# Performance work log

Hardware: AMD Instinct MI355X
Metric: run time of the kernel (lower is better)

## Reference

```python
import jax, jax.numpy as jnp
import numpy as np

R = 5.0  # public goods enhancement factor (init arg r)


def _neighbor_sum(x):
    # circular-padded conv2d with plus-shaped kernel [[0,1,0],[1,1,1],[0,1,0]]
    # == self + 4 von Neumann neighbors with wraparound
    return (x
            + jnp.roll(x, 1, axis=0) + jnp.roll(x, -1, axis=0)
            + jnp.roll(x, 1, axis=1) + jnp.roll(x, -1, axis=1))


def setup_inputs() -> dict:
    key = jax.random.key(0)
    ks = jax.random.split(key, 5)
    L, H = 2048, 64
    state = jax.random.randint(ks[0], (L, L), 0, 2, dtype=jnp.int32)
    s = 0.1
    return {
        "state": state,
        "W1": jax.random.normal(ks[1], (3, H), dtype=jnp.float32) * s,
        "b1": jnp.zeros((H,), dtype=jnp.float32),
        "W2": jax.random.normal(ks[2], (H, H), dtype=jnp.float32) * s,
        "b2": jnp.zeros((H,), dtype=jnp.float32),
        "Wa": jax.random.normal(ks[3], (H, 2), dtype=jnp.float32) * s,
        "ba": jnp.zeros((2,), dtype=jnp.float32),
        "Wc": jax.random.normal(ks[4], (H, 1), dtype=jnp.float32) * s,
        "bc": jnp.zeros((1,), dtype=jnp.float32),
    }


def reference(state, W1, b1, W2, b2, Wa, ba, Wc, bc):
    sf = state.astype(jnp.float32)                      # [L, L]

    # --- calculate_reward ---
    nc = _neighbor_sum(sf)                              # neighbor_coop [L, L]
    c_single = R * nc / 5.0 - 1.0
    d_single = R * nc / 5.0
    c_total = _neighbor_sum(c_single) + c_single
    d_total = _neighbor_sum(d_single) + d_single
    reward = jnp.where(state.astype(bool), c_total, d_total)  # [L, L]

    # --- encode_state ---
    global_coop = jnp.mean(sf)
    feats = jnp.stack(
        [sf, nc, jnp.broadcast_to(global_coop, sf.shape)], axis=-1
    ).reshape(-1, 3)                                    # [L*L, 3]

    # --- ActorCritic ---
    h = jax.nn.relu(feats @ W1 + b1)
    h = jax.nn.relu(h @ W2 + b2)
    action_probs = jax.nn.softmax(h @ Wa + ba, axis=-1)  # [L*L, 2]
    state_value = (h @ Wc + bc).squeeze(-1)              # [L*L]
    return action_probs, state_value, reward
```

## Files before the change

### kernel.cpp

```cpp
#include <hip/hip_runtime.h>
#include <math.h>

#define L 2048
#define LMASK (L - 1)
#define LB 512
#define LBMASK (LB - 1)
#define NCELL (L * L)
#define H 64

#define RED_BLOCKS 256
#define RED_THREADS 256
#define RED_ITERS (NCELL / 4 / (RED_BLOCKS * RED_THREADS))

__global__ void reduce_sum_kernel(const int* __restrict__ state,
                                  int* __restrict__ partials) {
    const int4* s4 = (const int4*)state;
    int tid = blockIdx.x * blockDim.x + threadIdx.x;
    int x = 0;
    #pragma unroll
    for (int k = 0; k < RED_ITERS; ++k) {
        int4 v = s4[tid + k * (RED_BLOCKS * RED_THREADS)];
        x += v.x + v.y + v.z + v.w;
    }
    #pragma unroll
    for (int off = 32; off > 0; off >>= 1)
        x += __shfl_down(x, off, 64);
    __shared__ int ls[4];
    if ((threadIdx.x & 63) == 0) ls[threadIdx.x >> 6] = x;
    __syncthreads();
    if (threadIdx.x == 0)
        partials[blockIdx.x] = ls[0] + ls[1] + ls[2] + ls[3];
}

__global__ void mlp_table_kernel(const float* __restrict__ W1,
                                 const float* __restrict__ b1,
                                 const float* __restrict__ W2,
                                 const float* __restrict__ b2,
                                 const float* __restrict__ Wa,
                                 const float* __restrict__ ba,
                                 const float* __restrict__ Wc,
                                 const float* __restrict__ bc,
                                 const int* __restrict__ partials,
                                 float* __restrict__ table) {
    __shared__ float h1[H];
    __shared__ float h2[H];
    int b = blockIdx.x;
    int j = threadIdx.x;

    int sum = partials[j] + partials[j + 64] + partials[j + 128] + partials[j + 192];
    #pragma unroll
    for (int off = 32; off > 0; off >>= 1)
        sum += __shfl_xor(sum, off, 64);

    float f0 = (float)(b / 6);
    float f1 = (float)(b % 6);
    float f2 = (float)sum * (1.0f / (float)NCELL);

    float a = W1[0 * H + j] * f0 + W1[1 * H + j] * f1 + W1[2 * H + j] * f2 + b1[j];
    h1[j] = fmaxf(a, 0.0f);
    __syncthreads();

    float acc = b2[j];
    #pragma unroll
    for (int k = 0; k < H; ++k) acc += h1[k] * W2[k * H + j];
    h2[j] = fmaxf(acc, 0.0f);
    __syncthreads();

    if (j == 0) {
        float la = ba[0], lb = ba[1], v = bc[0];
        #pragma unroll
        for (int k = 0; k < H; ++k) {
            la += h2[k] * Wa[k * 2 + 0];
            lb += h2[k] * Wa[k * 2 + 1];
            v  += h2[k] * Wc[k];
        }
        float m = fmaxf(la, lb);
        float e0 = expf(la - m), e1 = expf(lb - m);
        float inv = 1.0f / (e0 + e1);
        table[b * 4 + 0] = e0 * inv;
        table[b * 4 + 1] = e1 * inv;
        table[b * 4 + 2] = v;
    }
}

__global__ void cell_kernel(const int* __restrict__ state,
                            const float* __restrict__ table,
                            float* __restrict__ out) {
    __shared__ float tbl[48];
    if (threadIdx.x < 48) tbl[threadIdx.x] = table[threadIdx.x];
    __syncthreads();

    int tid = blockIdx.x * blockDim.x + threadIdx.x;
    int i  = tid >> 9;
    int jb = tid & LBMASK;
    int im1 = (i - 1) & LMASK, ip1 = (i + 1) & LMASK;
    int im2 = (i - 2) & LMASK, ip2 = (i + 2) & LMASK;
    int jbm1 = (jb - 1) & LBMASK, jbp1 = (jb + 1) & LBMASK;

    const int4* s4 = (const int4*)state;
    int4 m0 = s4[i   * LB + jbm1], m1 = s4[i   * LB + jb], m2 = s4[i   * LB + jbp1];
    int4 n0 = s4[im1 * LB + jbm1], n1 = s4[im1 * LB + jb], n2 = s4[im1 * LB + jbp1];
    int4 q0 = s4[ip1 * LB + jbm1], q1 = s4[ip1 * LB + jb], q2 = s4[ip1 * LB + jbp1];
    int4 uu4 = s4[im2 * LB + jb];
    int4 dd4 = s4[ip2 * LB + jb];

    int m [12] = {m0.x,m0.y,m0.z,m0.w, m1.x,m1.y,m1.z,m1.w, m2.x,m2.y,m2.z,m2.w};
    int nr[12] = {n0.x,n0.y,n0.z,n0.w, n1.x,n1.y,n1.z,n1.w, n2.x,n2.y,n2.z,n2.w};
    int sr[12] = {q0.x,q0.y,q0.z,q0.w, q1.x,q1.y,q1.z,q1.w, q2.x,q2.y,q2.z,q2.w};
    int ur[4]  = {uu4.x,uu4.y,uu4.z,uu4.w};
    int dr[4]  = {dd4.x,dd4.y,dd4.z,dd4.w};

    float pr[8], vv[4], rw[4];
    #pragma unroll
    for (int t = 0; t < 4; ++t) {
        int c  = m[4 + t],  w  = m[3 + t],  e  = m[5 + t];
        int ww = m[2 + t],  ee = m[6 + t];
        int n  = nr[4 + t], nw = nr[3 + t], ne = nr[5 + t];
        int s  = sr[4 + t], sw = sr[3 + t], se = sr[5 + t];
        int nn = ur[t],     ss = dr[t];

        int axis1 = n + s + e + w;
        rw[t] = (float)(3 * axis1 + 2 * (nw + ne + sw + se) + (nn + ss + ww + ee));

        int combo = c * 6 + (c + axis1);
        pr[2 * t]     = tbl[combo * 4 + 0];
        pr[2 * t + 1] = tbl[combo * 4 + 1];
        vv[t]         = tbl[combo * 4 + 2];
    }

    float4* o4 = (float4*)out;
    o4[tid * 2]     = make_float4(pr[0], pr[1], pr[2], pr[3]);
    o4[tid * 2 + 1] = make_float4(pr[4], pr[5], pr[6], pr[7]);
    ((float4*)(out + 2 * (size_t)NCELL))[tid] = make_float4(vv[0], vv[1], vv[2], vv[3]);
    ((float4*)(out + 3 * (size_t)NCELL))[tid] = make_float4(rw[0], rw[1], rw[2], rw[3]);
}

extern "C" void kernel_launch(void* const* d_in, const int* in_sizes, int n_in,
                              void* d_out, int out_size, void* d_ws, size_t ws_size,
                              hipStream_t stream) {
    const int*   state = (const int*)d_in[0];
    const float* W1 = (const float*)d_in[1];
    const float* b1 = (const float*)d_in[2];
    const float* W2 = (const float*)d_in[3];
    const float* b2 = (const float*)d_in[4];
    const float* Wa = (const float*)d_in[5];
    const float* ba = (const float*)d_in[6];
    const float* Wc = (const float*)d_in[7];
    const float* bc = (const float*)d_in[8];
    float* out = (float*)d_out;

    int*   partials = (int*)d_ws;
    float* table    = (float*)((char*)d_ws + 1024);

    reduce_sum_kernel<<<RED_BLOCKS, RED_THREADS, 0, stream>>>(state, partials);
    mlp_table_kernel<<<12, 64, 0, stream>>>(W1, b1, W2, b2, Wa, ba, Wc, bc,
                                            partials, table);
    cell_kernel<<<NCELL / 4 / 256, 256, 0, stream>>>(state, table, out);
}
```

Baseline: 116.4 us.

## Fuse MLP table computation into cell kernel and widen reduction grid

Removes the separate MLP-table kernel launch by having every cell-kernel block redundantly compute the 12-entry lookup table in shared memory from the reduction partials. The reduction grid grows from 256 to 1024 blocks to spread the global sum over more CUs. This saves one launch and a dependency gap, but each of the 4096 blocks now does about 50K FMAs of MLP work plus extra syncs before its stencil work.

```diff
diff --git a/kernel.cpp b/kernel.cpp
--- a/kernel.cpp
+++ b/kernel.cpp
@@ -7,10 +7,10 @@
 #define LBMASK (LB - 1)
 #define NCELL (L * L)
 #define H 64
+#define BLK 256
 
-#define RED_BLOCKS 256
-#define RED_THREADS 256
-#define RED_ITERS (NCELL / 4 / (RED_BLOCKS * RED_THREADS))
+#define RED_BLOCKS 1024
+#define RED_ITERS (NCELL / 4 / (RED_BLOCKS * BLK))
 
 __global__ void reduce_sum_kernel(const int* __restrict__ state,
                                   int* __restrict__ partials) {
@@ -19,7 +19,7 @@
     int x = 0;
     #pragma unroll
     for (int k = 0; k < RED_ITERS; ++k) {
-        int4 v = s4[tid + k * (RED_BLOCKS * RED_THREADS)];
+        int4 v = s4[tid + k * (RED_BLOCKS * BLK)];
         x += v.x + v.y + v.z + v.w;
     }
     #pragma unroll
@@ -32,65 +32,72 @@
         partials[blockIdx.x] = ls[0] + ls[1] + ls[2] + ls[3];
 }
 
-__global__ void mlp_table_kernel(const float* __restrict__ W1,
-                                 const float* __restrict__ b1,
-                                 const float* __restrict__ W2,
-                                 const float* __restrict__ b2,
-                                 const float* __restrict__ Wa,
-                                 const float* __restrict__ ba,
-                                 const float* __restrict__ Wc,
-                                 const float* __restrict__ bc,
-                                 const int* __restrict__ partials,
-                                 float* __restrict__ table) {
-    __shared__ float h1[H];
-    __shared__ float h2[H];
-    int b = blockIdx.x;
-    int j = threadIdx.x;
+__global__ __launch_bounds__(BLK)
+void cell_kernel(const int* __restrict__ state,
+                 const float* __restrict__ W1, const float* __restrict__ b1,
+                 const float* __restrict__ W2, const float* __restrict__ b2,
+                 const float* __restrict__ Wa, const float* __restrict__ ba,
+                 const float* __restrict__ Wc, const float* __restrict__ bc,
+                 const int* __restrict__ partials,
+                 float* __restrict__ out) {
+    __shared__ float tbl[48];
+    __shared__ float h1s[12][H];
+    __shared__ float h2s[12][H];
+    __shared__ int   ls[4];
+    __shared__ float gc_s;
 
-    int sum = partials[j] + partials[j + 64] + partials[j + 128] + partials[j + 192];
+    const int t = threadIdx.x;
+
+    int s = partials[t] + partials[t + 256] + partials[t + 512] + partials[t + 768];
     #pragma unroll
-    for (int off = 32; off > 0; off >>= 1)
-        sum += __shfl_xor(sum, off, 64);
+    for (int off = 32; off > 0; off >>= 1) s += __shfl_down(s, off, 64);
+    if ((t & 63) == 0) ls[t >> 6] = s;
+    __syncthreads();
+    if (t == 0) gc_s = (float)(ls[0] + ls[1] + ls[2] + ls[3]) * (1.0f / (float)NCELL);
+    __syncthreads();
+    const float gc = gc_s;
 
-    float f0 = (float)(b / 6);
-    float f1 = (float)(b % 6);
-    float f2 = (float)sum * (1.0f / (float)NCELL);
-
-    float a = W1[0 * H + j] * f0 + W1[1 * H + j] * f1 + W1[2 * H + j] * f2 + b1[j];
-    h1[j] = fmaxf(a, 0.0f);
+    const int cb = t >> 4;
+    const int kk = t & 15;
+    if (cb < 12) {
+        float f0 = (float)(cb / 6), f1 = (float)(cb % 6);
+        #pragma unroll
+        for (int d = 0; d < 4; ++d) {
+            int j = kk * 4 + d;
+            float a = W1[j] * f0 + W1[H + j] * f1 + W1[2 * H + j] * gc + b1[j];
+            h1s[cb][j] = fmaxf(a, 0.f);
+        }
+    }
     __syncthreads();
-
-    float acc = b2[j];
-    #pragma unroll
-    for (int k = 0; k < H; ++k) acc += h1[k] * W2[k * H + j];
-    h2[j] = fmaxf(acc, 0.0f);
+    if (cb < 12) {
+        #pragma unroll
+        for (int d = 0; d < 4; ++d) {
+            int j = kk * 4 + d;
+            float acc = b2[j];
+            #pragma unroll 8
+            for (int q = 0; q < H; ++q) acc += h1s[cb][q] * W2[q * H + j];
+            h2s[cb][j] = fmaxf(acc, 0.f);
+        }
+    }
     __syncthreads();
-
-    if (j == 0) {
+    if (t < 12) {
         float la = ba[0], lb = ba[1], v = bc[0];
-        #pragma unroll
-        for (int k = 0; k < H; ++k) {
-            la += h2[k] * Wa[k * 2 + 0];
-            lb += h2[k] * Wa[k * 2 + 1];
-            v  += h2[k] * Wc[k];
+        #pragma unroll 8
+        for (int q = 0; q < H; ++q) {
+            la += h2s[t][q] * Wa[q * 2 + 0];
+            lb += h2s[t][q] * Wa[q * 2 + 1];
+            v  += h2s[t][q] * Wc[q];
         }
         float m = fmaxf(la, lb);
         float e0 = expf(la - m), e1 = expf(lb - m);
-        float inv = 1.0f / (e0 + e1);
-        table[b * 4 + 0] = e0 * inv;
-        table[b * 4 + 1] = e1 * inv;
-        table[b * 4 + 2] = v;
+        float inv = 1.f / (e0 + e1);
+        tbl[t * 4 + 0] = e0 * inv;
+        tbl[t * 4 + 1] = e1 * inv;
+        tbl[t * 4 + 2] = v;
     }
-}
-
-__global__ void cell_kernel(const int* __restrict__ state,
-                            const float* __restrict__ table,
-                            float* __restrict__ out) {
-    __shared__ float tbl[48];
-    if (threadIdx.x < 48) tbl[threadIdx.x] = table[threadIdx.x];
     __syncthreads();
 
-    int tid = blockIdx.x * blockDim.x + threadIdx.x;
+    int tid = blockIdx.x * BLK + t;
     int i  = tid >> 9;
     int jb = tid & LBMASK;
     int im1 = (i - 1) & LMASK, ip1 = (i + 1) & LMASK;
@@ -112,25 +119,25 @@
 
     float pr[8], vv[4], rw[4];
     #pragma unroll
-    for (int t = 0; t < 4; ++t) {
-        int c  = m[4 + t],  w  = m[3 + t],  e  = m[5 + t];
-        int ww = m[2 + t],  ee = m[6 + t];
-        int n  = nr[4 + t], nw = nr[3 + t], ne = nr[5 + t];
-        int s  = sr[4 + t], sw = sr[3 + t], se = sr[5 + t];
-        int nn = ur[t],     ss = dr[t];
+    for (int u = 0; u < 4; ++u) {
+        int c  = m[4 + u],  w  = m[3 + u],  e  = m[5 + u];
+        int ww = m[2 + u],  ee = m[6 + u];
+        int n  = nr[4 + u], nw = nr[3 + u], ne = nr[5 + u];
+        int ss1 = sr[4 + u], sw = sr[3 + u], se = sr[5 + u];
+        int nn = ur[u],     ssd = dr[u];
 
-        int axis1 = n + s + e + w;
-        rw[t] = (float)(3 * axis1 + 2 * (nw + ne + sw + se) + (nn + ss + ww + ee));
+        int axis1 = n + ss1 + e + w;
+        rw[u] = (float)(3 * axis1 + 2 * (nw + ne + sw + se) + (nn + ssd + ww + ee));
 
         int combo = c * 6 + (c + axis1);
-        pr[2 * t]     = tbl[combo * 4 + 0];
-        pr[2 * t + 1] = tbl[combo * 4 + 1];
-        vv[t]         = tbl[combo * 4 + 2];
+        pr[2 * u]     = tbl[combo * 4 + 0];
+        pr[2 * u + 1] = tbl[combo * 4 + 1];
+        vv[u]         = tbl[combo * 4 + 2];
     }
 
     float4* o4 = (float4*)out;
-    o4[tid * 2]     = make_float4(pr[0], pr[1], pr[2], pr[3]);
-    o4[tid * 2 + 1] = make_float4(pr[4], pr[5], pr[6], pr[7]);
+    o4[(size_t)tid * 2]     = make_float4(pr[0], pr[1], pr[2], pr[3]);
+    o4[(size_t)tid * 2 + 1] = make_float4(pr[4], pr[5], pr[6], pr[7]);
     ((float4*)(out + 2 * (size_t)NCELL))[tid] = make_float4(vv[0], vv[1], vv[2], vv[3]);
     ((float4*)(out + 3 * (size_t)NCELL))[tid] = make_float4(rw[0], rw[1], rw[2], rw[3]);
 }
@@ -149,11 +156,10 @@
     const float* bc = (const float*)d_in[8];
     float* out = (float*)d_out;
 
-    int*   partials = (int*)d_ws;
-    float* table    = (float*)((char*)d_ws + 1024);
+    int* partials = (int*)d_ws;
 
-    reduce_sum_kernel<<<RED_BLOCKS, RED_THREADS, 0, stream>>>(state, partials);
-    mlp_table_kernel<<<12, 64, 0, stream>>>(W1, b1, W2, b2, Wa, ba, Wc, bc,
-                                            partials, table);
-    cell_kernel<<<NCELL / 4 / 256, 256, 0, stream>>>(state, table, out);
+    reduce_sum_kernel<<<RED_BLOCKS, BLK, 0, stream>>>(state, partials);
+    cell_kernel<<<NCELL / 4 / BLK, BLK, 0, stream>>>(state, W1, b1, W2, b2,
+                                                     Wa, ba, Wc, bc,
+                                                     partials, out);
 }
```

New measurement: 275.5 us. +136.7%, slower.

## Widen reduction grid, remap cell blocks across XCDs, use nontemporal output stores

Applied to the files above, without the earlier changes.

Raises the reduction grid from 256 to 1024 blocks so more CUs share the first pass, and widens the partial-sum gather and workspace offset to match. Remaps cell-kernel block indices so consecutive rows land on the same XCD, which is meant to improve L2 reuse of neighbouring stencil rows. Writes the large output arrays with nontemporal stores to avoid polluting cache with write-once data. The remap assumes the grid divides evenly by 8 and that hardware dispatches blocks round-robin across XCDs.

```diff
diff --git a/kernel.cpp b/kernel.cpp
--- a/kernel.cpp
+++ b/kernel.cpp
@@ -7,10 +7,12 @@
 #define LBMASK (LB - 1)
 #define NCELL (L * L)
 #define H 64
+#define BLK 256
 
-#define RED_BLOCKS 256
-#define RED_THREADS 256
-#define RED_ITERS (NCELL / 4 / (RED_BLOCKS * RED_THREADS))
+#define RED_BLOCKS 1024
+#define RED_ITERS (NCELL / 4 / (RED_BLOCKS * BLK))
+
+typedef float vfloat4 __attribute__((ext_vector_type(4)));
 
 __global__ void reduce_sum_kernel(const int* __restrict__ state,
                                   int* __restrict__ partials) {
@@ -19,7 +21,7 @@
     int x = 0;
     #pragma unroll
     for (int k = 0; k < RED_ITERS; ++k) {
-        int4 v = s4[tid + k * (RED_BLOCKS * RED_THREADS)];
+        int4 v = s4[tid + k * (RED_BLOCKS * BLK)];
         x += v.x + v.y + v.z + v.w;
     }
     #pragma unroll
@@ -47,7 +49,10 @@
     int b = blockIdx.x;
     int j = threadIdx.x;
 
-    int sum = partials[j] + partials[j + 64] + partials[j + 128] + partials[j + 192];
+    int sum = 0;
+    #pragma unroll
+    for (int k = 0; k < RED_BLOCKS / 64; ++k)
+        sum += partials[k * 64 + j];
     #pragma unroll
     for (int off = 32; off > 0; off >>= 1)
         sum += __shfl_xor(sum, off, 64);
@@ -83,14 +88,19 @@
     }
 }
 
-__global__ void cell_kernel(const int* __restrict__ state,
-                            const float* __restrict__ table,
-                            float* __restrict__ out) {
+#define NXCD 8
+#define GRID3 (NCELL / 4 / BLK)
+__global__ __launch_bounds__(BLK)
+void cell_kernel(const int* __restrict__ state,
+                 const float* __restrict__ table,
+                 float* __restrict__ out) {
     __shared__ float tbl[48];
     if (threadIdx.x < 48) tbl[threadIdx.x] = table[threadIdx.x];
     __syncthreads();
 
-    int tid = blockIdx.x * blockDim.x + threadIdx.x;
+    int blk = (blockIdx.x & (NXCD - 1)) * (GRID3 / NXCD) + (blockIdx.x >> 3);
+
+    int tid = blk * BLK + threadIdx.x;
     int i  = tid >> 9;
     int jb = tid & LBMASK;
     int im1 = (i - 1) & LMASK, ip1 = (i + 1) & LMASK;
@@ -112,27 +122,31 @@
 
     float pr[8], vv[4], rw[4];
     #pragma unroll
-    for (int t = 0; t < 4; ++t) {
-        int c  = m[4 + t],  w  = m[3 + t],  e  = m[5 + t];
-        int ww = m[2 + t],  ee = m[6 + t];
-        int n  = nr[4 + t], nw = nr[3 + t], ne = nr[5 + t];
-        int s  = sr[4 + t], sw = sr[3 + t], se = sr[5 + t];
-        int nn = ur[t],     ss = dr[t];
+    for (int u = 0; u < 4; ++u) {
+        int c  = m[4 + u],  w  = m[3 + u],  e  = m[5 + u];
+        int ww = m[2 + u],  ee = m[6 + u];
+        int n  = nr[4 + u], nw = nr[3 + u], ne = nr[5 + u];
+        int s  = sr[4 + u], sw = sr[3 + u], se = sr[5 + u];
+        int nn = ur[u],     ss = dr[u];
 
         int axis1 = n + s + e + w;
-        rw[t] = (float)(3 * axis1 + 2 * (nw + ne + sw + se) + (nn + ss + ww + ee));
+        rw[u] = (float)(3 * axis1 + 2 * (nw + ne + sw + se) + (nn + ss + ww + ee));
 
         int combo = c * 6 + (c + axis1);
-        pr[2 * t]     = tbl[combo * 4 + 0];
-        pr[2 * t + 1] = tbl[combo * 4 + 1];
-        vv[t]         = tbl[combo * 4 + 2];
+        pr[2 * u]     = tbl[combo * 4 + 0];
+        pr[2 * u + 1] = tbl[combo * 4 + 1];
+        vv[u]         = tbl[combo * 4 + 2];
     }
 
-    float4* o4 = (float4*)out;
-    o4[tid * 2]     = make_float4(pr[0], pr[1], pr[2], pr[3]);
-    o4[tid * 2 + 1] = make_float4(pr[4], pr[5], pr[6], pr[7]);
-    ((float4*)(out + 2 * (size_t)NCELL))[tid] = make_float4(vv[0], vv[1], vv[2], vv[3]);
-    ((float4*)(out + 3 * (size_t)NCELL))[tid] = make_float4(rw[0], rw[1], rw[2], rw[3]);
+    vfloat4* o4 = (vfloat4*)out;
+    vfloat4 s0 = {pr[0], pr[1], pr[2], pr[3]};
+    vfloat4 s1 = {pr[4], pr[5], pr[6], pr[7]};
+    vfloat4 s2 = {vv[0], vv[1], vv[2], vv[3]};
+    vfloat4 s3 = {rw[0], rw[1], rw[2], rw[3]};
+    __builtin_nontemporal_store(s0, &o4[(size_t)tid * 2]);
+    __builtin_nontemporal_store(s1, &o4[(size_t)tid * 2 + 1]);
+    __builtin_nontemporal_store(s2, &((vfloat4*)(out + 2 * (size_t)NCELL))[tid]);
+    __builtin_nontemporal_store(s3, &((vfloat4*)(out + 3 * (size_t)NCELL))[tid]);
 }
 
 extern "C" void kernel_launch(void* const* d_in, const int* in_sizes, int n_in,
@@ -150,10 +164,10 @@
     float* out = (float*)d_out;
 
     int*   partials = (int*)d_ws;
-    float* table    = (float*)((char*)d_ws + 1024);
+    float* table    = (float*)((char*)d_ws + 8192);
 
-    reduce_sum_kernel<<<RED_BLOCKS, RED_THREADS, 0, stream>>>(state, partials);
+    reduce_sum_kernel<<<RED_BLOCKS, BLK, 0, stream>>>(state, partials);
     mlp_table_kernel<<<12, 64, 0, stream>>>(W1, b1, W2, b2, Wa, ba, Wc, bc,
                                             partials, table);
-    cell_kernel<<<NCELL / 4 / 256, 256, 0, stream>>>(state, table, out);
+    cell_kernel<<<GRID3, BLK, 0, stream>>>(state, table, out);
 }
```

New measurement: 119.6 us. +2.7%, slower.
